# Kernel optimization log

Hardware: AMD Instinct MI355X
Metric: run time of the kernel (lower is better)

The kernel has to match this reference:

```python
import jax, jax.numpy as jnp
import numpy as np

RES_UP_RATIO = 0.05   # reserve_up_ratio (mgr.args default)
RES_DN_RATIO = 0.02   # reserve_dn_ratio
REQ_UP_RATIO = 0.02   # system_reserve_up_ratio
REQ_DN_RATIO = 0.02   # system_reserve_dn_ratio


def _build_K(G):
    """Static constraint matrix of the per-timestep LP over x=[P, R_up, R_dn] (n=3G).
    Row 0 is the equality sum(P)=D; remaining rows are <= inequalities."""
    n = 3 * G
    m = 1 + 4 * G + 2
    K = np.zeros((m, n), dtype=np.float32)
    I = np.eye(G, dtype=np.float32)
    K[0, :G] = 1.0                      # sum_g P = D
    r = 1
    K[r:r+G, :G] = I;  K[r:r+G, G:2*G] = I;  r += G      # P + R_up <= pmax
    K[r:r+G, :G] = -I; K[r:r+G, 2*G:3*G] = I; r += G     # -P + R_dn <= -pmin
    K[r:r+G, :G] = I;  r += G                             # P <= pmax
    K[r:r+G, :G] = -I; r += G                             # -P <= -pmin
    K[r, G:2*G] = -1.0; r += 1                            # -sum R_up <= -req_up*D
    K[r, 2*G:3*G] = -1.0                                  # -sum R_dn <= -req_dn*D
    return K


def _solve_da_lp(forecast, pmin, pmax, b, n_iters):
    """Batched PDHG (Chambolle-Pock) solve of all B*T per-timestep LPs.
    Returns P, R_up, R_dn with shape (B, T, G)."""
    B, T = forecast.shape
    G = b.shape[0]
    Knp = _build_K(G)
    L = float(np.linalg.norm(Knp, 2))          # static spectral norm of K
    tau = sigma = 0.9 / L
    K = jnp.asarray(Knp)
    m, n = K.shape
    # objective coefficients over x=[P, R_up, R_dn] (Cost = b*P + c is affine)
    c_obj = jnp.concatenate([b, RES_UP_RATIO * b, RES_DN_RATIO * b])  # (n,)
    # rhs q: (B, T, m)
    q = jnp.concatenate([
        forecast[..., None],
        jnp.broadcast_to(pmax, (B, T, G)),
        jnp.broadcast_to(-pmin, (B, T, G)),
        jnp.broadcast_to(pmax, (B, T, G)),
        jnp.broadcast_to(-pmin, (B, T, G)),
        -REQ_UP_RATIO * forecast[..., None],
        -REQ_DN_RATIO * forecast[..., None],
    ], axis=-1)
    ineq = (jnp.arange(m) > 0)  # row 0 = equality dual (unprojected)

    x0 = jnp.zeros((B, T, n), dtype=forecast.dtype)
    y0 = jnp.zeros((B, T, m), dtype=forecast.dtype)

    def step(carry, _):
        x, y = carry
        x_new = jnp.maximum(x - tau * (c_obj + jnp.einsum('btm,mn->btn', y, K)), 0.0)
        x_bar = 2.0 * x_new - x
        y_new = y + sigma * (jnp.einsum('btn,mn->btm', x_bar, K) - q)
        y_new = jnp.where(ineq, jnp.maximum(y_new, 0.0), y_new)
        return (x_new, y_new), None

    (x, _), _ = jax.lax.scan(step, (x0, y0), None, length=n_iters)
    P = x[..., :G]
    Ru = x[..., G:2*G]
    Rd = x[..., 2*G:3*G]
    return P, Ru, Rd


def setup_inputs() -> dict:
    key = jax.random.key(0)
    k1, k2, k3, k4 = jax.random.split(key, 4)
    G, B, T = 50, 128, 24
    pmax = 100.0 + 400.0 * jax.random.uniform(k1, (G,), dtype=jnp.float32)
    pmin = 0.1 * pmax
    b = 20.0 + 30.0 * jax.random.uniform(k2, (G,), dtype=jnp.float32)
    c = 100.0 * jax.random.uniform(k3, (G,), dtype=jnp.float32)
    lo, hi = jnp.sum(pmin), jnp.sum(pmax)
    # feasible demand: comfortably inside [sum pmin, sum pmax] so reserves exist
    forecast = lo + (0.35 + 0.3 * jax.random.uniform(k4, (B, T), dtype=jnp.float32)) * (hi - lo)
    return {"forecast": forecast, "pmin": pmin, "pmax": pmax, "b": b, "c": c, "n_iters": 300}


def reference(forecast, pmin, pmax, b, c, n_iters):
    P, Ru, Rd = _solve_da_lp(forecast, pmin, pmax, b, n_iters)  # (B,T,G)
    # match torch layout (B, G, T)
    P_DA = jnp.swapaxes(P, 1, 2)
    R_up = jnp.swapaxes(Ru, 1, 2)
    R_dn = jnp.swapaxes(Rd, 1, 2)
    Cost_DA = b[None, :, None] * P_DA + c[None, :, None]
    ru_price = (RES_UP_RATIO * b)[None, :, None]
    rd_price = (RES_DN_RATIO * b)[None, :, None]
    obj = Cost_DA.sum((1, 2)) + (ru_price * R_up).sum((1, 2)) + (rd_price * R_dn).sum((1, 2))
    return (P_DA, R_up, R_dn, obj, Cost_DA)
```

## Files before the change

### kernel.cpp

```cpp
#include <hip/hip_runtime.h>
#include <math.h>

#define G   50
#define T   24
#define B   128
#define NLP (B * T)
#define SZ  (B * G * T)

typedef float v2f __attribute__((ext_vector_type(2)));


__device__ __forceinline__ v2f vmax0(v2f v) {
    v2f z = {0.f, 0.f};
    return __builtin_elementwise_max(v, z);
}

template <int CTRL>
__device__ __forceinline__ float dpp_mov(float x) {
    int r = __builtin_amdgcn_update_dpp(0, __float_as_int(x), CTRL, 0xf, 0xf, true);
    return __int_as_float(r);
}

__device__ __forceinline__ void row_sum3(float& a, float& b, float& c) {
    a += dpp_mov<0x121>(a); b += dpp_mov<0x121>(b); c += dpp_mov<0x121>(c);
    a += dpp_mov<0x122>(a); b += dpp_mov<0x122>(b); c += dpp_mov<0x122>(c);
    a += dpp_mov<0x124>(a); b += dpp_mov<0x124>(b); c += dpp_mov<0x124>(c);
    a += dpp_mov<0x128>(a); b += dpp_mov<0x128>(b); c += dpp_mov<0x128>(c);
}

__device__ __forceinline__ float row_sum1(float a) {
    a += dpp_mov<0x121>(a);
    a += dpp_mov<0x122>(a);
    a += dpp_mov<0x124>(a);
    a += dpp_mov<0x128>(a);
    return a;
}

__global__ __launch_bounds__(64)
void pdhg_lp_kernel(const float* __restrict__ forecast,
                    const float* __restrict__ pmin,
                    const float* __restrict__ pmax,
                    const float* __restrict__ bcost,
                    const float* __restrict__ ccost,
                    const int*   __restrict__ n_iters_p,
                    float* __restrict__ out,
                    float* __restrict__ ws_partial,
                    float tau)
{
    const int lane = threadIdx.x;
    const int lh   = lane & 15;
    const int row  = lane >> 4;
    const int lp   = blockIdx.x * 4 + row;
    const int b    = lp / T;
    const int t    = lp - b * T;
    const int n_iters = n_iters_p[0];

    const int  gA0 = lh,      gA1 = lh + 16;
    const int  gB0 = lh + 32;
    const int  gB1 = lh + 48;
    const bool vB1 = (lh < 2);

    v2f bjA  = { bcost[gA0], bcost[gA1] };
    v2f bjB  = { bcost[gB0], vB1 ? bcost[gB1] : 0.f };
    v2f cjA  = { ccost[gA0], ccost[gA1] };
    v2f cjB  = { ccost[gB0], vB1 ? ccost[gB1] : 0.f };
    v2f pmxA = { pmax[gA0],  pmax[gA1] };
    v2f pmxB = { pmax[gB0],  vB1 ? pmax[gB1] : 0.f };
    v2f pmnA = { pmin[gA0],  pmin[gA1] };
    v2f pmnB = { pmin[gB0],  vB1 ? pmin[gB1] : 0.f };
    const float f = forecast[lp];

    const float ts  = tau * tau;
    const float BIG = 1e30f;

    v2f tcPA  = tau * bjA;
    v2f tcPB  = tau * bjB;           if (!vB1) tcPB.y  = BIG;
    v2f tcRuA = (tau * 0.05f) * bjA;
    v2f tcRuB = (tau * 0.05f) * bjB; if (!vB1) tcRuB.y = BIG;
    v2f tcRdA = (tau * 0.02f) * bjA;
    v2f tcRdB = (tau * 0.02f) * bjB; if (!vB1) tcRdB.y = BIG;
    v2f tspmxA = ts * pmxA, tspmxB = ts * pmxB;
    v2f tspmnA = ts * pmnA, tspmnB = ts * pmnB;
    const float tsf   = ts * f;
    const float tsreq = ts * 0.02f * f;

    v2f PA = {0,0}, PB = {0,0}, RuA = {0,0}, RuB = {0,0}, RdA = {0,0}, RdB = {0,0};
    v2f z1A = {0,0}, z1B = {0,0}, z2A = {0,0}, z2B = {0,0};
    v2f z3A = {0,0}, z3B = {0,0}, z4A = {0,0}, z4B = {0,0};
    float z0 = 0.f, zru = 0.f, zrd = 0.f;

    for (int it = 0; it < n_iters; ++it) {
        v2f z0v = { z0, z0 };
        v2f zruv = { zru, zru };
        v2f zrdv = { zrd, zrd };
        v2f gPA = (z1A - z2A) + (z3A - z4A) + z0v;
        v2f gPB = (z1B - z2B) + (z3B - z4B) + z0v;
        v2f PnA = vmax0(PA - tcPA - gPA);
        v2f PnB = vmax0(PB - tcPB - gPB);
        v2f RunA = vmax0(RuA - tcRuA - z1A + zruv);
        v2f RunB = vmax0(RuB - tcRuB - z1B + zruv);
        v2f RdnA = vmax0(RdA - tcRdA - z2A + zrdv);
        v2f RdnB = vmax0(RdB - tcRdB - z2B + zrdv);

        v2f PbA  = 2.f * PnA  - PA,  PbB  = 2.f * PnB  - PB;
        v2f RubA = 2.f * RunA - RuA, RubB = 2.f * RunB - RuB;
        v2f RdbA = 2.f * RdnA - RdA, RdbB = 2.f * RdnB - RdB;
        PA = PnA; PB = PnB; RuA = RunA; RuB = RunB; RdA = RdnA; RdB = RdnB;

        v2f tP = PbA + PbB, tRu = RubA + RubB, tRd = RdbA + RdbB;
        float sP  = tP.x  + tP.y;
        float sRu = tRu.x + tRu.y;
        float sRd = tRd.x + tRd.y;
        row_sum3(sP, sRu, sRd);

        z0  = z0 + ts * sP - tsf;
        z1A = vmax0(z1A + ts * (PbA + RubA) - tspmxA);
        z1B = vmax0(z1B + ts * (PbB + RubB) - tspmxB);
        z2A = vmax0(z2A + ts * (RdbA - PbA) + tspmnA);
        z2B = vmax0(z2B + ts * (RdbB - PbB) + tspmnB);
        z3A = vmax0(z3A + ts * PbA - tspmxA);
        z3B = vmax0(z3B + ts * PbB - tspmxB);
        z4A = vmax0(z4A - ts * PbA + tspmnA);
        z4B = vmax0(z4B - ts * PbB + tspmnB);
        zru = fmaxf(zru + tsreq - ts * sRu, 0.f);
        zrd = fmaxf(zrd + tsreq - ts * sRd, 0.f);
    }

    const v2f costA = bjA * PA + cjA;
    const v2f costB = bjB * PB + cjB;
    {
        const int bgt = b * (G * T) + t;
        const int a0 = bgt + gA0 * T, a1 = bgt + gA1 * T, b0 = bgt + gB0 * T;
        out[a0] = PA.x;  out[SZ + a0] = RuA.x;  out[2*SZ + a0] = RdA.x;  out[3*SZ + B + a0] = costA.x;
        out[a1] = PA.y;  out[SZ + a1] = RuA.y;  out[2*SZ + a1] = RdA.y;  out[3*SZ + B + a1] = costA.y;
        out[b0] = PB.x;  out[SZ + b0] = RuB.x;  out[2*SZ + b0] = RdB.x;  out[3*SZ + B + b0] = costB.x;
        if (vB1) {
            const int b1 = bgt + gB1 * T;
            out[b1] = PB.y;  out[SZ + b1] = RuB.y;  out[2*SZ + b1] = RdB.y;  out[3*SZ + B + b1] = costB.y;
        }
    }

    if (ws_partial) {
        v2f lo = costA + (0.05f * bjA) * RuA + (0.02f * bjA) * RdA
               + costB + (0.05f * bjB) * RuB + (0.02f * bjB) * RdB;
        float tot = row_sum1(lo.x + lo.y);
        if (lh == 0) ws_partial[lp] = tot;
    }
}

__global__ __launch_bounds__(64)
void obj_final_kernel(const float* __restrict__ ws_partial, float* __restrict__ out)
{
    const int b = blockIdx.x * 64 + threadIdx.x;
    if (b < B) {
        float s = 0.f;
        #pragma unroll
        for (int t = 0; t < T; ++t) s += ws_partial[b * T + t];
        out[3 * SZ + b] = s;
    }
}

__global__ __launch_bounds__(256)
void obj_kernel(const float* __restrict__ bcost, float* __restrict__ out)
{
    const int b = blockIdx.x;
    const float* Ru = out + SZ     + (size_t)b * (G * T);
    const float* Rd = out + 2 * SZ + (size_t)b * (G * T);
    const float* C  = out + 3 * SZ + B + (size_t)b * (G * T);

    float s = 0.f;
    for (int i = threadIdx.x; i < G * T; i += 256) {
        const int g = i / T;
        const float bg = bcost[g];
        s += C[i] + 0.05f * bg * Ru[i] + 0.02f * bg * Rd[i];
    }
    __shared__ float sm[16];
    s = row_sum1(s);
    if ((threadIdx.x & 15) == 0) sm[threadIdx.x >> 4] = s;
    __syncthreads();
    if (threadIdx.x == 0) {
        float tot = 0.f;
        #pragma unroll
        for (int i = 0; i < 16; ++i) tot += sm[i];
        out[3 * SZ + b] = tot;
    }
}

extern "C" void kernel_launch(void* const* d_in, const int* in_sizes, int n_in,
                              void* d_out, int out_size, void* d_ws, size_t ws_size,
                              hipStream_t stream) {
    const float* forecast = (const float*)d_in[0];
    const float* pmin_p   = (const float*)d_in[1];
    const float* pmax_p   = (const float*)d_in[2];
    const float* b_p      = (const float*)d_in[3];
    const float* c_p      = (const float*)d_in[4];
    const int*   niter_p  = (const int*)  d_in[5];
    float* out = (float*)d_out;

    const double L = sqrt((105.0 + sqrt(17.0)) * 0.5);
    const float tau = (float)(0.9 / L);

    const bool use_ws = (ws_size >= (size_t)NLP * sizeof(float));
    float* wsp = use_ws ? (float*)d_ws : nullptr;

    pdhg_lp_kernel<<<NLP / 4, 64, 0, stream>>>(forecast, pmin_p, pmax_p,
                                               b_p, c_p, niter_p, out, wsp, tau);
    if (use_ws) {
        obj_final_kernel<<<(B + 63) / 64, 64, 0, stream>>>(wsp, out);
    } else {
        obj_kernel<<<B, 256, 0, stream>>>(b_p, out);
    }
}
```

Before: 137.9 us.

## Use packed f32 inline asm in PDHG loop and fuse objective via atomics

```diff
diff --git a/kernel.cpp b/kernel.cpp
--- a/kernel.cpp
+++ b/kernel.cpp
@@ -10,6 +10,21 @@
 typedef float v2f __attribute__((ext_vector_type(2)));
 
 
+__device__ __forceinline__ v2f pk_add(v2f a, v2f b) {
+    v2f d; asm("v_pk_add_f32 %0, %1, %2" : "=v"(d) : "v"(a), "v"(b)); return d;
+}
+__device__ __forceinline__ v2f pk_sub(v2f a, v2f b) {
+    v2f d; asm("v_pk_add_f32 %0, %1, %2 neg_lo:[0,1] neg_hi:[0,1]"
+               : "=v"(d) : "v"(a), "v"(b)); return d;
+}
+__device__ __forceinline__ v2f pk_fma(v2f a, v2f b, v2f c) {
+    v2f d; asm("v_pk_fma_f32 %0, %1, %2, %3" : "=v"(d) : "v"(a), "v"(b), "v"(c));
+    return d;
+}
+__device__ __forceinline__ v2f pk_fms(v2f a, v2f b, v2f c) {
+    v2f d; asm("v_pk_fma_f32 %0, %1, %2, %3 neg_lo:[0,0,1] neg_hi:[0,0,1]"
+               : "=v"(d) : "v"(a), "v"(b), "v"(c)); return d;
+}
 __device__ __forceinline__ v2f vmax0(v2f v) {
     v2f z = {0.f, 0.f};
     return __builtin_elementwise_max(v, z);
@@ -27,7 +42,6 @@
     a += dpp_mov<0x124>(a); b += dpp_mov<0x124>(b); c += dpp_mov<0x124>(c);
     a += dpp_mov<0x128>(a); b += dpp_mov<0x128>(b); c += dpp_mov<0x128>(c);
 }
-
 __device__ __forceinline__ float row_sum1(float a) {
     a += dpp_mov<0x121>(a);
     a += dpp_mov<0x122>(a);
@@ -44,7 +58,6 @@
                     const float* __restrict__ ccost,
                     const int*   __restrict__ n_iters_p,
                     float* __restrict__ out,
-                    float* __restrict__ ws_partial,
                     float tau)
 {
     const int lane = threadIdx.x;
@@ -73,6 +86,10 @@
     const float ts  = tau * tau;
     const float BIG = 1e30f;
 
+    const v2f tsv  = { ts, ts };
+    const v2f ntsv = { -ts, -ts };
+    const v2f twov = { 2.f, 2.f };
+
     v2f tcPA  = tau * bjA;
     v2f tcPB  = tau * bjB;           if (!vB1) tcPB.y  = BIG;
     v2f tcRuA = (tau * 0.05f) * bjA;
@@ -90,40 +107,44 @@
     float z0 = 0.f, zru = 0.f, zrd = 0.f;
 
     for (int it = 0; it < n_iters; ++it) {
-        v2f z0v = { z0, z0 };
-        v2f zruv = { zru, zru };
-        v2f zrdv = { zrd, zrd };
-        v2f gPA = (z1A - z2A) + (z3A - z4A) + z0v;
-        v2f gPB = (z1B - z2B) + (z3B - z4B) + z0v;
-        v2f PnA = vmax0(PA - tcPA - gPA);
-        v2f PnB = vmax0(PB - tcPB - gPB);
-        v2f RunA = vmax0(RuA - tcRuA - z1A + zruv);
-        v2f RunB = vmax0(RuB - tcRuB - z1B + zruv);
-        v2f RdnA = vmax0(RdA - tcRdA - z2A + zrdv);
-        v2f RdnB = vmax0(RdB - tcRdB - z2B + zrdv);
+        const v2f z0v  = { z0,  z0  };
+        const v2f zruv = { zru, zru };
+        const v2f zrdv = { zrd, zrd };
 
-        v2f PbA  = 2.f * PnA  - PA,  PbB  = 2.f * PnB  - PB;
-        v2f RubA = 2.f * RunA - RuA, RubB = 2.f * RunB - RuB;
-        v2f RdbA = 2.f * RdnA - RdA, RdbB = 2.f * RdnB - RdB;
+        v2f gPA = pk_add(pk_add(pk_sub(z1A, z2A), pk_sub(z3A, z4A)), z0v);
+        v2f gPB = pk_add(pk_add(pk_sub(z1B, z2B), pk_sub(z3B, z4B)), z0v);
+        v2f PnA = vmax0(pk_sub(PA, pk_add(tcPA, gPA)));
+        v2f PnB = vmax0(pk_sub(PB, pk_add(tcPB, gPB)));
+        v2f RunA = vmax0(pk_sub(pk_add(RuA, zruv), pk_add(z1A, tcRuA)));
+        v2f RunB = vmax0(pk_sub(pk_add(RuB, zruv), pk_add(z1B, tcRuB)));
+        v2f RdnA = vmax0(pk_sub(pk_add(RdA, zrdv), pk_add(z2A, tcRdA)));
+        v2f RdnB = vmax0(pk_sub(pk_add(RdB, zrdv), pk_add(z2B, tcRdB)));
+
+        v2f PbA  = pk_fms(PnA,  twov, PA);
+        v2f PbB  = pk_fms(PnB,  twov, PB);
+        v2f RubA = pk_fms(RunA, twov, RuA);
+        v2f RubB = pk_fms(RunB, twov, RuB);
+        v2f RdbA = pk_fms(RdnA, twov, RdA);
+        v2f RdbB = pk_fms(RdnB, twov, RdB);
         PA = PnA; PB = PnB; RuA = RunA; RuB = RunB; RdA = RdnA; RdB = RdnB;
 
-        v2f tP = PbA + PbB, tRu = RubA + RubB, tRd = RdbA + RdbB;
+        v2f tP = pk_add(PbA, PbB), tRu = pk_add(RubA, RubB), tRd = pk_add(RdbA, RdbB);
         float sP  = tP.x  + tP.y;
         float sRu = tRu.x + tRu.y;
         float sRd = tRd.x + tRd.y;
         row_sum3(sP, sRu, sRd);
 
-        z0  = z0 + ts * sP - tsf;
-        z1A = vmax0(z1A + ts * (PbA + RubA) - tspmxA);
-        z1B = vmax0(z1B + ts * (PbB + RubB) - tspmxB);
-        z2A = vmax0(z2A + ts * (RdbA - PbA) + tspmnA);
-        z2B = vmax0(z2B + ts * (RdbB - PbB) + tspmnB);
-        z3A = vmax0(z3A + ts * PbA - tspmxA);
-        z3B = vmax0(z3B + ts * PbB - tspmxB);
-        z4A = vmax0(z4A - ts * PbA + tspmnA);
-        z4B = vmax0(z4B - ts * PbB + tspmnB);
-        zru = fmaxf(zru + tsreq - ts * sRu, 0.f);
-        zrd = fmaxf(zrd + tsreq - ts * sRd, 0.f);
+        z0 = fmaf(ts, sP, z0 - tsf);
+        z1A = vmax0(pk_fma(tsv, pk_add(PbA, RubA), pk_sub(z1A, tspmxA)));
+        z1B = vmax0(pk_fma(tsv, pk_add(PbB, RubB), pk_sub(z1B, tspmxB)));
+        z2A = vmax0(pk_fma(tsv, pk_sub(RdbA, PbA), pk_add(z2A, tspmnA)));
+        z2B = vmax0(pk_fma(tsv, pk_sub(RdbB, PbB), pk_add(z2B, tspmnB)));
+        z3A = vmax0(pk_fma(tsv,  PbA, pk_sub(z3A, tspmxA)));
+        z3B = vmax0(pk_fma(tsv,  PbB, pk_sub(z3B, tspmxB)));
+        z4A = vmax0(pk_fma(ntsv, PbA, pk_add(z4A, tspmnA)));
+        z4B = vmax0(pk_fma(ntsv, PbB, pk_add(z4B, tspmnB)));
+        zru = fmaxf(fmaf(-ts, sRu, zru + tsreq), 0.f);
+        zrd = fmaxf(fmaf(-ts, sRd, zrd + tsreq), 0.f);
     }
 
     const v2f costA = bjA * PA + cjA;
@@ -140,49 +161,11 @@
         }
     }
 
-    if (ws_partial) {
+    {
         v2f lo = costA + (0.05f * bjA) * RuA + (0.02f * bjA) * RdA
                + costB + (0.05f * bjB) * RuB + (0.02f * bjB) * RdB;
         float tot = row_sum1(lo.x + lo.y);
-        if (lh == 0) ws_partial[lp] = tot;
-    }
-}
-
-__global__ __launch_bounds__(64)
-void obj_final_kernel(const float* __restrict__ ws_partial, float* __restrict__ out)
-{
-    const int b = blockIdx.x * 64 + threadIdx.x;
-    if (b < B) {
-        float s = 0.f;
-        #pragma unroll
-        for (int t = 0; t < T; ++t) s += ws_partial[b * T + t];
-        out[3 * SZ + b] = s;
-    }
-}
-
-__global__ __launch_bounds__(256)
-void obj_kernel(const float* __restrict__ bcost, float* __restrict__ out)
-{
-    const int b = blockIdx.x;
-    const float* Ru = out + SZ     + (size_t)b * (G * T);
-    const float* Rd = out + 2 * SZ + (size_t)b * (G * T);
-    const float* C  = out + 3 * SZ + B + (size_t)b * (G * T);
-
-    float s = 0.f;
-    for (int i = threadIdx.x; i < G * T; i += 256) {
-        const int g = i / T;
-        const float bg = bcost[g];
-        s += C[i] + 0.05f * bg * Ru[i] + 0.02f * bg * Rd[i];
-    }
-    __shared__ float sm[16];
-    s = row_sum1(s);
-    if ((threadIdx.x & 15) == 0) sm[threadIdx.x >> 4] = s;
-    __syncthreads();
-    if (threadIdx.x == 0) {
-        float tot = 0.f;
-        #pragma unroll
-        for (int i = 0; i < 16; ++i) tot += sm[i];
-        out[3 * SZ + b] = tot;
+        if (lh == 0) atomicAdd(&out[3 * SZ + b], tot);
     }
 }
 
@@ -200,14 +183,8 @@
     const double L = sqrt((105.0 + sqrt(17.0)) * 0.5);
     const float tau = (float)(0.9 / L);
 
-    const bool use_ws = (ws_size >= (size_t)NLP * sizeof(float));
-    float* wsp = use_ws ? (float*)d_ws : nullptr;
+    hipMemsetAsync(out + 3 * SZ, 0, B * sizeof(float), stream);
 
     pdhg_lp_kernel<<<NLP / 4, 64, 0, stream>>>(forecast, pmin_p, pmax_p,
-                                               b_p, c_p, niter_p, out, wsp, tau);
-    if (use_ws) {
-        obj_final_kernel<<<(B + 63) / 64, 64, 0, stream>>>(wsp, out);
-    } else {
-        obj_kernel<<<B, 256, 0, stream>>>(b_p, out);
-    }
+                                               b_p, c_p, niter_p, out, tau);
 }
```

Result: slower. 155.1 us (+12.5%).
